# Kernel tuning notes

Hardware: AMD Instinct MI355X
Metric: run time of the kernel (lower is better)

The kernel has to match this reference:

```python
import jax, jax.numpy as jnp
import numpy as np

B, N, C, H = 16, 207, 64, 64

def setup_inputs() -> dict:
    key = jax.random.key(0)
    k1, k2, k3, k4, k5 = jax.random.split(key, 5)
    return {
        "x": jax.random.normal(k1, (B, N, C), dtype=jnp.float32),
        "state": jax.random.normal(k2, (B, N, 1, H), dtype=jnp.float32),
        "Wx": jax.random.normal(k3, (B, N, C, 3 * H), dtype=jnp.float32) * 0.1,
        "Wh": jax.random.normal(k4, (B, N, H, 3 * H), dtype=jnp.float32) * 0.1,
        "b": jax.random.normal(k5, (B, N, 1, 3 * H), dtype=jnp.float32) * 0.1,
    }

def reference(x, state, Wx, Wh, b):
    # x: [B,N,C] -> [B,N,1,C]; state (h): [B,N,1,H]
    if x.ndim == 3:
        x = x[..., None, :]
    h = state
    dim_hidden = Wh.shape[-2]
    # One fused batched matmul for x @ Wx, then split into r/z/c parts.
    xW = jnp.matmul(x, Wx)  # [B,N,1,3H]
    xr, xz, xc = jnp.split(xW, 3, axis=-1)
    Wrh, Wzh, Wch = jnp.split(Wh, 3, axis=-1)
    br, bz, bc = jnp.split(b, 3, axis=-1)
    r = jax.nn.sigmoid(xr + jnp.matmul(h, Wrh) + br)
    z = jax.nn.sigmoid(xz + jnp.matmul(h, Wzh) + bz)
    # Note torch precedence: r * h @ Wch == (r * h) @ Wch
    hc = jnp.tanh(xc + jnp.matmul(r * h, Wch) + bc)
    h_new = (1.0 - z) * h + z * hc  # [B,N,1,H]
    return h_new
```

## Files before the change

### kernel.cpp

```cpp
#include <hip/hip_runtime.h>
#include <math.h>


#define GC 64
#define GH 64
#define J3 192
#define WPP (GC * J3)

typedef float f4 __attribute__((ext_vector_type(4)));

__global__ __launch_bounds__(256, 8) void gru_cell_v6(
    const float* __restrict__ x,
    const float* __restrict__ state,
    const float* __restrict__ Wx,
    const float* __restrict__ Wh,
    const float* __restrict__ b,
    float* __restrict__ out)
{
    const int pos = blockIdx.x;
    const int t = threadIdx.x;

    __shared__ float x_s[GC];
    __shared__ float mult_s[2 * GH];
    __shared__ float part[1024];
    __shared__ float z_s[GH];

    if (t < GC)           x_s[t]          = x[(size_t)pos * GC + t];
    else if (t < GC + GH) mult_s[t - GC]  = state[(size_t)pos * GH + (t - GC)];
    __syncthreads();

    const f4* __restrict__ Wx4 = (const f4*)(Wx + (size_t)pos * WPP);
    const f4* __restrict__ Wh4 = (const f4*)(Wh + (size_t)pos * WPP);

    {
        const int jg = t & 15;
        const int rp = t >> 4;
        f4 acc = {0.f, 0.f, 0.f, 0.f};
        #pragma unroll
        for (int k = 0; k < 4; ++k) {
            const int c = rp + 16 * k;
            const f4 wx4 = __builtin_nontemporal_load(Wx4 + c * 48 + jg);
            const f4 wh4 = __builtin_nontemporal_load(Wh4 + c * 48 + jg);
            const float xs = x_s[c];
            const float hs = mult_s[c];
            acc.x += xs * wx4.x + hs * wh4.x;
            acc.y += xs * wx4.y + hs * wh4.y;
            acc.z += xs * wx4.z + hs * wh4.z;
            acc.w += xs * wx4.w + hs * wh4.w;
        }
        *((f4*)&part[rp * 64 + 4 * jg]) = acc;
    }
    __syncthreads();

    if (t < GH) {
        float v = b[(size_t)pos * J3 + t];
        #pragma unroll
        for (int rp = 0; rp < 16; ++rp) v += part[rp * 64 + t];
        const float r = 1.f / (1.f + expf(-v));
        mult_s[GH + t] = r * mult_s[t];
    }
    __syncthreads();

    float vc = 0.f;
    {
        const int jg = t & 31;
        const int rp = t >> 5;
        const int msel = (jg & 16) << 2;
        f4 acc = {0.f, 0.f, 0.f, 0.f};
        #pragma unroll 4
        for (int k = 0; k < 8; ++k) {
            const int c = rp + 8 * k;
            const f4 wx4 = __builtin_nontemporal_load(Wx4 + c * 48 + 16 + jg);
            const f4 wh4 = __builtin_nontemporal_load(Wh4 + c * 48 + 16 + jg);
            const float xs = x_s[c];
            const float ms = mult_s[msel + c];
            acc.x += xs * wx4.x + ms * wh4.x;
            acc.y += xs * wx4.y + ms * wh4.y;
            acc.z += xs * wx4.z + ms * wh4.z;
            acc.w += xs * wx4.w + ms * wh4.w;
        }
        *((f4*)&part[rp * 128 + 4 * jg]) = acc;
    }
    __syncthreads();

    if (t < 2 * GH) {
        float v = b[(size_t)pos * J3 + GH + t];
        #pragma unroll
        for (int rp = 0; rp < 8; ++rp) v += part[rp * 128 + t];
        if (t < GH) z_s[t] = 1.f / (1.f + expf(-v));
        else        vc = v;
    }
    __syncthreads();

    if (t >= GH && t < 2 * GH) {
        const int j = t - GH;
        const float hc = tanhf(vc);
        const float z = z_s[j];
        out[(size_t)pos * GH + j] = (1.f - z) * mult_s[j] + z * hc;
    }
}

extern "C" void kernel_launch(void* const* d_in, const int* in_sizes, int n_in,
                              void* d_out, int out_size, void* d_ws, size_t ws_size,
                              hipStream_t stream) {
    const float* x     = (const float*)d_in[0];
    const float* state = (const float*)d_in[1];
    const float* Wx    = (const float*)d_in[2];
    const float* Wh    = (const float*)d_in[3];
    const float* b     = (const float*)d_in[4];
    float* out = (float*)d_out;

    const int npos = in_sizes[0] / GC;

    gru_cell_v6<<<npos, 256, 0, stream>>>(x, state, Wx, Wh, b, out);
}
```

Baseline: 316.8 us.

## Issue five of six weight loads before the r-gate barrier and broadcast inputs via shuffles

Restructures the GRU cell so each thread loads the r, z and x-part of c weights in the first phase, leaving only the Wh c-slice for after the r gate is known. Input x and h values are broadcast with wave shuffles instead of shared memory, and bias loads are hoisted to the start. The aim is to put more of the memory-bound weight stream in flight before the first barrier and to drop one sync stage. In exchange each thread holds more live registers and the shared partial buffer doubles in size.

```diff
diff --git a/kernel.cpp b/kernel.cpp
--- a/kernel.cpp
+++ b/kernel.cpp
@@ -9,7 +9,11 @@
 
 typedef float f4 __attribute__((ext_vector_type(4)));
 
-__global__ __launch_bounds__(256, 8) void gru_cell_v6(
+__device__ __forceinline__ float sigm(float v) {
+    return 1.f / (1.f + expf(-v));
+}
+
+__global__ __launch_bounds__(256, 8) void gru_cell_v7(
     const float* __restrict__ x,
     const float* __restrict__ state,
     const float* __restrict__ Wx,
@@ -17,86 +21,87 @@
     const float* __restrict__ b,
     float* __restrict__ out)
 {
-    const int pos = blockIdx.x;
-    const int t = threadIdx.x;
+    const int pos  = blockIdx.x;
+    const int t    = threadIdx.x;
+    const int lane = t & 63;
 
-    __shared__ float x_s[GC];
-    __shared__ float mult_s[2 * GH];
-    __shared__ float part[1024];
+    __shared__ float rh_s[GH];
     __shared__ float z_s[GH];
+    __shared__ float part[16 * 128];
 
-    if (t < GC)           x_s[t]          = x[(size_t)pos * GC + t];
-    else if (t < GC + GH) mult_s[t - GC]  = state[(size_t)pos * GH + (t - GC)];
-    __syncthreads();
+    const float xv = x[(size_t)pos * GC + lane];
+    const float hv = state[(size_t)pos * GH + lane];
+    float bA = 0.f, bC = 0.f;
+    if (t < 128) bA = b[(size_t)pos * J3 + t];
+    if (t < 64)  bC = b[(size_t)pos * J3 + 128 + t];
 
     const f4* __restrict__ Wx4 = (const f4*)(Wx + (size_t)pos * WPP);
     const f4* __restrict__ Wh4 = (const f4*)(Wh + (size_t)pos * WPP);
 
-    {
-        const int jg = t & 15;
-        const int rp = t >> 4;
-        f4 acc = {0.f, 0.f, 0.f, 0.f};
+    const int jg = t & 15;
+    const int rp = t >> 4;
+
+    f4 accR = {0.f,0.f,0.f,0.f};
+    f4 accZ = {0.f,0.f,0.f,0.f};
+    f4 accC = {0.f,0.f,0.f,0.f};
+
+    #pragma unroll
+    for (int k = 0; k < 4; ++k) {
+        const int c = rp + 16 * k;
+        const int base = c * 48 + jg;
+        const f4 wxr = __builtin_nontemporal_load(Wx4 + base);
+        const f4 wxz = __builtin_nontemporal_load(Wx4 + base + 16);
+        const f4 wxc = __builtin_nontemporal_load(Wx4 + base + 32);
+        const f4 whr = __builtin_nontemporal_load(Wh4 + base);
+        const f4 whz = __builtin_nontemporal_load(Wh4 + base + 16);
+        const float xs = __shfl(xv, c);
+        const float hs = __shfl(hv, c);
+        accR.x += xs * wxr.x + hs * whr.x;
+        accR.y += xs * wxr.y + hs * whr.y;
+        accR.z += xs * wxr.z + hs * whr.z;
+        accR.w += xs * wxr.w + hs * whr.w;
+        accZ.x += xs * wxz.x + hs * whz.x;
+        accZ.y += xs * wxz.y + hs * whz.y;
+        accZ.z += xs * wxz.z + hs * whz.z;
+        accZ.w += xs * wxz.w + hs * whz.w;
+        accC.x += xs * wxc.x;
+        accC.y += xs * wxc.y;
+        accC.z += xs * wxc.z;
+        accC.w += xs * wxc.w;
+    }
+    *((f4*)&part[rp * 128 + 4 * jg])      = accR;
+    *((f4*)&part[rp * 128 + 64 + 4 * jg]) = accZ;
+    __syncthreads();
+
+    if (t < 128) {
+        float v = bA;
         #pragma unroll
-        for (int k = 0; k < 4; ++k) {
-            const int c = rp + 16 * k;
-            const f4 wx4 = __builtin_nontemporal_load(Wx4 + c * 48 + jg);
-            const f4 wh4 = __builtin_nontemporal_load(Wh4 + c * 48 + jg);
-            const float xs = x_s[c];
-            const float hs = mult_s[c];
-            acc.x += xs * wx4.x + hs * wh4.x;
-            acc.y += xs * wx4.y + hs * wh4.y;
-            acc.z += xs * wx4.z + hs * wh4.z;
-            acc.w += xs * wx4.w + hs * wh4.w;
-        }
-        *((f4*)&part[rp * 64 + 4 * jg]) = acc;
+        for (int p = 0; p < 16; ++p) v += part[p * 128 + t];
+        if (t < 64) rh_s[t]      = sigm(v) * hv;
+        else        z_s[t - 64]  = sigm(v);
     }
     __syncthreads();
 
-    if (t < GH) {
-        float v = b[(size_t)pos * J3 + t];
-        #pragma unroll
-        for (int rp = 0; rp < 16; ++rp) v += part[rp * 64 + t];
-        const float r = 1.f / (1.f + expf(-v));
-        mult_s[GH + t] = r * mult_s[t];
+    #pragma unroll
+    for (int k = 0; k < 4; ++k) {
+        const int c = rp + 16 * k;
+        const f4 whc = __builtin_nontemporal_load(Wh4 + c * 48 + 32 + jg);
+        const float rs = rh_s[c];
+        accC.x += rs * whc.x;
+        accC.y += rs * whc.y;
+        accC.z += rs * whc.z;
+        accC.w += rs * whc.w;
     }
+    *((f4*)&part[rp * 64 + 4 * jg]) = accC;
     __syncthreads();
 
-    float vc = 0.f;
-    {
-        const int jg = t & 31;
-        const int rp = t >> 5;
-        const int msel = (jg & 16) << 2;
-        f4 acc = {0.f, 0.f, 0.f, 0.f};
-        #pragma unroll 4
-        for (int k = 0; k < 8; ++k) {
-            const int c = rp + 8 * k;
-            const f4 wx4 = __builtin_nontemporal_load(Wx4 + c * 48 + 16 + jg);
-            const f4 wh4 = __builtin_nontemporal_load(Wh4 + c * 48 + 16 + jg);
-            const float xs = x_s[c];
-            const float ms = mult_s[msel + c];
-            acc.x += xs * wx4.x + ms * wh4.x;
-            acc.y += xs * wx4.y + ms * wh4.y;
-            acc.z += xs * wx4.z + ms * wh4.z;
-            acc.w += xs * wx4.w + ms * wh4.w;
-        }
-        *((f4*)&part[rp * 128 + 4 * jg]) = acc;
-    }
-    __syncthreads();
-
-    if (t < 2 * GH) {
-        float v = b[(size_t)pos * J3 + GH + t];
+    if (t < 64) {
+        float v = bC;
         #pragma unroll
-        for (int rp = 0; rp < 8; ++rp) v += part[rp * 128 + t];
-        if (t < GH) z_s[t] = 1.f / (1.f + expf(-v));
-        else        vc = v;
-    }
-    __syncthreads();
-
-    if (t >= GH && t < 2 * GH) {
-        const int j = t - GH;
-        const float hc = tanhf(vc);
-        const float z = z_s[j];
-        out[(size_t)pos * GH + j] = (1.f - z) * mult_s[j] + z * hc;
+        for (int p = 0; p < 16; ++p) v += part[p * 64 + t];
+        const float hc = tanhf(v);
+        const float z  = z_s[t];
+        out[(size_t)pos * GH + t] = (1.f - z) * hv + z * hc;
     }
 }
 
@@ -112,5 +117,5 @@
 
     const int npos = in_sizes[0] / GC;
 
-    gru_cell_v6<<<npos, 256, 0, stream>>>(x, state, Wx, Wh, b, out);
+    gru_cell_v7<<<npos, 256, 0, stream>>>(x, state, Wx, Wh, b, out);
 }
```

Result: faster. 308.2 us (-2.7%).
